# Kernel optimization log

Measured on AMD Instinct MI355X. Metric: run time of the kernel, lower is better.

## Reference

```python
import jax, jax.numpy as jnp
import numpy as np

V, D, K, NB, T = 50257, 128, 3, 8, 64
DIV_W = 2.0  # diversity_weight


def setup_inputs() -> dict:
    key = jax.random.key(0)
    k1, k2, k3 = jax.random.split(key, 3)
    tokens = jax.random.randint(k1, (T,), 0, V)
    E = jax.random.normal(k2, (V, D), jnp.float32)          # embedding table
    bubbles = 1.5 * jax.random.normal(k3, (K, NB, D), jnp.float32)  # init_spread_foam scale=1.5
    decay_base = jnp.asarray(0.8, jnp.float32)
    sensitivity = jnp.asarray(1.0, jnp.float32)
    return {"tokens": tokens, "E": E, "bubbles": bubbles,
            "decay_base": decay_base, "sensitivity": sensitivity}


def reference(tokens, E, bubbles, decay_base, sensitivity):
    d = E.shape[1]
    inv_sqrt_d = 1.0 / jnp.sqrt(jnp.asarray(d, jnp.float32))
    # normalized bubble states (pure-state directions), fixed over time
    psi = bubbles / (jnp.linalg.norm(bubbles, axis=-1, keepdims=True) + 1e-10)  # [K,NB,D]

    def step(memories, tok):
        # memories: [K, NB, D]
        x = E[tok]  # [D]
        mem_mean = memories.mean(axis=1)  # [K, D]
        mem_norm = jnp.linalg.norm(mem_mean, axis=-1) + 1e-10  # [K]
        x_norm = jnp.linalg.norm(x) + 1e-10
        cos = (mem_mean @ x) / (x_norm * mem_norm)  # [K]
        novelty = jnp.where(mem_norm > 1e-8, 1.0 - cos, 1.0)  # [K]
        decay = jax.nn.sigmoid(decay_base - jnp.abs(sensitivity) * novelty)  # [K]
        xm = x[None, :] + decay[:, None] * mem_mean  # [K, D]

        # foam forward (vectorized over K foams)
        scores = DIV_W * jnp.einsum('knd,kd->kn', bubbles, xm) * inv_sqrt_d  # [K,NB]
        w = jax.nn.softmax(scores, axis=-1)  # [K,NB]
        rho_k = jnp.einsum('kn,knd,kne->kde', w, psi, psi)  # [K,D,D] PSD, trace 1
        eq = w[..., None] * xm[:, None, :] + (1.0 - w)[..., None] * bubbles  # [K,NB,D]
        new_mem = decay[:, None, None] * memories + (1.0 - decay)[:, None, None] * eq

        rho = rho_k.mean(axis=0)  # [D,D] ensemble mixture
        eigs = jnp.clip(jnp.linalg.eigvalsh(rho), 1e-12)
        eigs = eigs / eigs.sum()
        logits = jnp.einsum('vd,de,ve->v', E, rho, E)  # born rule, [V]
        token_probs = jax.nn.softmax(logits)
        S_rho = -(eigs * jnp.clip(jnp.log(eigs), -100.0)).sum()
        H_tokens = -(token_probs * jnp.clip(jnp.log(token_probs), -100.0)).sum()
        F_tokens = H_tokens - S_rho
        logits_k = jnp.einsum('vd,kde,ve->kv', E, rho_k, E)  # [K,V]
        per_foam_probs = jax.nn.softmax(logits_k, axis=-1)
        return new_mem, (token_probs, rho, S_rho, H_tokens, F_tokens, per_foam_probs)

    mem0 = jnp.zeros((bubbles.shape[0], bubbles.shape[1], E.shape[1]), E.dtype)
    _, outs = jax.lax.scan(step, mem0, tokens)
    # outs: token_probs [T,V], rho [T,D,D], S_rho [T], H_tokens [T], F_tokens [T], per_foam_probs [T,K,V]
    return outs
```

## Files before the change

kernel.cpp:

```cpp
#include <hip/hip_runtime.h>
#include <math.h>

namespace {
constexpr int Vv  = 50257;
constexpr int Dc  = 128;
constexpr int Kc  = 3;
constexpr int NBc = 8;
constexpr int Jc  = 24;
constexpr int Tc  = 64;
constexpr int CHV = 1024;
constexpr int NCH = (Vv + CHV - 1) / CHV;
constexpr float INV_SQRT_D = 0.08838834764831845f;
constexpr float DIVW = 2.0f;

constexpr size_t WS_PSI  = 0;
constexpr size_t WS_G    = 4096;
constexpr size_t WS_BB   = 5120;
constexpr size_t WS_XN   = 6144;
constexpr size_t WS_BX   = 6400;
constexpr size_t WS_WALL = 8192;
constexpr size_t WS_PART = 12288;
constexpr size_t WS_LOGZ = 45056;
constexpr size_t WS_P2T  = 65536;

constexpr size_t OFF_TOK = 0;
constexpr size_t OFF_RHO = (size_t)Tc * Vv;
constexpr size_t OFF_S   = OFF_RHO + (size_t)Tc * Dc * Dc;
constexpr size_t OFF_H   = OFF_S + Tc;
constexpr size_t OFF_F   = OFF_H + Tc;
constexpr size_t OFF_PF  = OFF_F + Tc;
}

__device__ __forceinline__ float wsum64(float v) {
#pragma unroll
  for (int m = 1; m < 64; m <<= 1) v += __shfl_xor(v, m);
  return v;
}

__device__ __forceinline__ void comb(float& m1, float& s1, float m2, float s2) {
  float M = fmaxf(m1, m2);
  float e1 = (s1 > 0.f) ? expf(m1 - M) : 0.f;
  float e2 = (s2 > 0.f) ? expf(m2 - M) : 0.f;
  s1 = s1 * e1 + s2 * e2;
  m1 = M;
}
__device__ __forceinline__ void comb_sl(float& m1, float& s1, float& sl1,
                                        float m2, float s2, float sl2) {
  float M = fmaxf(m1, m2);
  float e1 = (s1 > 0.f) ? expf(m1 - M) : 0.f;
  float e2 = (s2 > 0.f) ? expf(m2 - M) : 0.f;
  s1 = s1 * e1 + s2 * e2;
  sl1 = sl1 * e1 + sl2 * e2;
  m1 = M;
}

__global__ void k_prep(const float* __restrict__ bub, float* __restrict__ ws) {
  __shared__ float braw[Jc * Dc];
  __shared__ float psi[Jc * Dc];
  __shared__ float nrm[Jc];
  int tid = threadIdx.x;
  for (int i = tid; i < Jc * Dc; i += 256) braw[i] = bub[i];
  __syncthreads();
  if (tid < Jc) {
    float s = 0.f;
    for (int d = 0; d < Dc; ++d) { float b = braw[tid * Dc + d]; s += b * b; }
    nrm[tid] = sqrtf(s) + 1e-10f;
  }
  __syncthreads();
  for (int i = tid; i < Jc * Dc; i += 256) {
    float v = braw[i] / nrm[i / Dc];
    psi[i] = v;
    ws[WS_PSI + i] = v;
  }
  __syncthreads();
  for (int i = tid; i < Jc * Jc; i += 256) {
    int r = i / Jc, c = i % Jc;
    float g = 0.f, b = 0.f;
    for (int d = 0; d < Dc; ++d) {
      g += psi[r * Dc + d] * psi[c * Dc + d];
      b += braw[r * Dc + d] * braw[c * Dc + d];
    }
    ws[WS_G + i] = g;
    ws[WS_BB + i] = b;
  }
}

__global__ void k_tok(const int* __restrict__ tok, const float* __restrict__ E,
                      const float* __restrict__ bub, float* __restrict__ ws) {
  int t = blockIdx.x, lane = threadIdx.x;
  int tk = tok[t];
  float eA = E[(size_t)tk * Dc + lane];
  float eB = E[(size_t)tk * Dc + 64 + lane];
  float xn = wsum64(eA * eA + eB * eB);
  if (lane == 0) ws[WS_XN + t] = xn;
  float p[Jc];
#pragma unroll
  for (int j = 0; j < Jc; ++j)
    p[j] = bub[j * Dc + lane] * eA + bub[j * Dc + 64 + lane] * eB;
#pragma unroll
  for (int j = 0; j < Jc; ++j) p[j] = wsum64(p[j]);
  if (lane == 0) {
#pragma unroll
    for (int j = 0; j < Jc; ++j) ws[WS_BX + (size_t)t * Jc + j] = p[j];
  }
}

__global__ void k_recur(const int* __restrict__ tok, const float* __restrict__ E,
                        const float* __restrict__ bub, const float* __restrict__ pdb,
                        const float* __restrict__ psn, float* __restrict__ ws) {
  __shared__ float sBX[Tc * Jc];
  __shared__ float sXN[Tc];
  int lane = threadIdx.x;
  for (int i = lane; i < Tc * Jc; i += 64) sBX[i] = ws[WS_BX + i];
  if (lane < Tc) sXN[lane] = ws[WS_XN + lane];
  float db = pdb[0];
  float sens = fabsf(psn[0]);
  int tokv = tok[lane];
  float bubA[Jc], bubB[Jc];
#pragma unroll
  for (int j = 0; j < Jc; ++j) {
    bubA[j] = bub[j * Dc + lane];
    bubB[j] = bub[j * Dc + 64 + lane];
  }
  int jme = (lane < Jc) ? lane : (Jc - 1);
  int kme = jme >> 3;
  float BBrow[Jc];
#pragma unroll
  for (int j = 0; j < Jc; ++j) BBrow[j] = ws[WS_BB + (size_t)jme * Jc + j];
  __syncthreads();
  float mmA[Kc] = {0.f, 0.f, 0.f}, mmB[Kc] = {0.f, 0.f, 0.f};
  float BMv[Kc] = {0.f, 0.f, 0.f};
  int tk0 = __shfl(tokv, 0);
  float xA = E[(size_t)tk0 * Dc + lane];
  float xB = E[(size_t)tk0 * Dc + 64 + lane];
  for (int t = 0; t < Tc; ++t) {
    float nxA = 0.f, nxB = 0.f;
    if (t + 1 < Tc) {
      int nk = __shfl(tokv, t + 1);
      nxA = E[(size_t)nk * Dc + lane];
      nxB = E[(size_t)nk * Dc + 64 + lane];
    }
    float dk[Kc], nk2[Kc];
#pragma unroll
    for (int k = 0; k < Kc; ++k) {
      dk[k]  = wsum64(mmA[k] * xA + mmB[k] * xB);
      nk2[k] = wsum64(mmA[k] * mmA[k] + mmB[k] * mmB[k]);
    }
    float xn = sqrtf(sXN[t]) + 1e-10f;
    float dec[Kc], xmA[Kc], xmB[Kc];
#pragma unroll
    for (int k = 0; k < Kc; ++k) {
      float mn = sqrtf(nk2[k]) + 1e-10f;
      float cosv = dk[k] / (xn * mn);
      float nov = (mn > 1e-8f) ? (1.f - cosv) : 1.f;
      dec[k] = 1.f / (1.f + expf(-(db - sens * nov)));
      xmA[k] = xA + dec[k] * mmA[k];
      xmB[k] = xB + dec[k] * mmB[k];
    }
    float bxj = sBX[t * Jc + jme];
    float decS = (kme == 0) ? dec[0] : ((kme == 1) ? dec[1] : dec[2]);
    float sc = (bxj + decS * BMv[kme]) * (DIVW * INV_SQRT_D);
    float mx = sc;
    mx = fmaxf(mx, __shfl_xor(mx, 1));
    mx = fmaxf(mx, __shfl_xor(mx, 2));
    mx = fmaxf(mx, __shfl_xor(mx, 4));
    float e = expf(sc - mx);
    float ss = e;
    ss += __shfl_xor(ss, 1);
    ss += __shfl_xor(ss, 2);
    ss += __shfl_xor(ss, 4);
    float w = e / ss;
    if (lane < Jc) ws[WS_WALL + (size_t)t * Jc + lane] = w;
    float wj[Jc];
#pragma unroll
    for (int j = 0; j < Jc; ++j) wj[j] = __shfl(w, j);
#pragma unroll
    for (int k = 0; k < Kc; ++k) {
      float accA = 0.f, accB = 0.f;
#pragma unroll
      for (int n = 0; n < NBc; ++n) {
        float om = 1.f - wj[k * NBc + n];
        accA += om * bubA[k * NBc + n];
        accB += om * bubB[k * NBc + n];
      }
      float od8 = (1.f - dec[k]) * 0.125f;
      mmA[k] = dec[k] * mmA[k] + od8 * (xmA[k] + accA);
      mmB[k] = dec[k] * mmB[k] + od8 * (xmB[k] + accB);
    }
#pragma unroll
    for (int k = 0; k < Kc; ++k) {
      float bxm = bxj + dec[k] * BMv[k];
      float s2 = 0.f;
#pragma unroll
      for (int n = 0; n < NBc; ++n) s2 += (1.f - wj[k * NBc + n]) * BBrow[k * NBc + n];
      BMv[k] = dec[k] * BMv[k] + (1.f - dec[k]) * 0.125f * (bxm + s2);
    }
    xA = nxA; xB = nxB;
  }
}

__global__ void k_proj(const float* __restrict__ E, float* __restrict__ ws) {
  __shared__ float4 psi4[Jc][Dc / 4];
  int tid = threadIdx.x;
  for (int i = tid; i < Jc * Dc / 4; i += 256)
    ((float4*)psi4)[i] = ((const float4*)(ws + WS_PSI))[i];
  __syncthreads();
  int v = blockIdx.x * 256 + tid;
  if (v >= Vv) return;
  float acc[Jc];
#pragma unroll
  for (int j = 0; j < Jc; ++j) acc[j] = 0.f;
  const float4* e4 = (const float4*)(E + (size_t)v * Dc);
  for (int d = 0; d < Dc / 4; ++d) {
    float4 e = e4[d];
#pragma unroll
    for (int j = 0; j < Jc; ++j) {
      float4 p = psi4[j][d];
      acc[j] += e.x * p.x + e.y * p.y + e.z * p.z + e.w * p.w;
    }
  }
#pragma unroll
  for (int j = 0; j < Jc; ++j) ws[WS_P2T + (size_t)j * Vv + v] = acc[j] * acc[j];
}

__global__ void k_rho(const float* __restrict__ ws, float* __restrict__ out) {
  int t = blockIdx.x;
  __shared__ float psis[Jc * Dc];
  __shared__ float wsh[Jc];
  int tid = threadIdx.x;
  for (int i = tid; i < Jc * Dc; i += 256) psis[i] = ws[WS_PSI + i];
  if (tid < Jc) wsh[tid] = ws[WS_WALL + (size_t)t * Jc + tid] * (1.f / 3.f);
  __syncthreads();
  int d = tid >> 1, eh = (tid & 1) * 64;
  float4 acc[16];
#pragma unroll
  for (int i = 0; i < 16; ++i) acc[i] = make_float4(0.f, 0.f, 0.f, 0.f);
  for (int j = 0; j < Jc; ++j) {
    float a = wsh[j] * psis[j * Dc + d];
    const float4* pr = (const float4*)&psis[j * Dc + eh];
#pragma unroll
    for (int i = 0; i < 16; ++i) {
      float4 p = pr[i];
      acc[i].x += a * p.x; acc[i].y += a * p.y; acc[i].z += a * p.z; acc[i].w += a * p.w;
    }
  }
  float* o = out + OFF_RHO + (size_t)t * Dc * Dc + (size_t)d * Dc + eh;
#pragma unroll
  for (int i = 0; i < 16; ++i) ((float4*)o)[i] = acc[i];
}

__global__ void k_eig(const float* __restrict__ ws, float* __restrict__ out) {
  int t = blockIdx.x;
  __shared__ float A[Jc * 25];
  int lane = threadIdx.x;
  for (int i = lane; i < Jc * Jc; i += 64) {
    int r = i / Jc, c = i % Jc;
    A[r * 25 + c] = ws[WS_G + i] *
                    sqrtf(ws[WS_WALL + (size_t)t * Jc + r] * ws[WS_WALL + (size_t)t * Jc + c]) *
                    (1.f / 3.f);
  }
  __syncthreads();
  for (int sweep = 0; sweep < 7; ++sweep) {
    for (int rr = 0; rr < 23; ++rr) {
      float cv = 1.f, sv = 0.f;
      if (lane < Jc) {
        int j = lane;
        int m = (j == 23) ? rr : ((j == rr) ? 23 : (2 * rr + 23 - j) % 23);
        int lo = min(j, m), hi = max(j, m);
        float ajj = A[j * 25 + j];
        float alh = A[lo * 25 + hi];
        float amm = __shfl(ajj, m);
        float app = (j == lo) ? ajj : amm;
        float aqq = (j == lo) ? amm : ajj;
        if (fabsf(alh) > 1e-20f) {
          float th = (aqq - app) / (2.f * alh);
          float tt = 1.f / (fabsf(th) + sqrtf(1.f + th * th));
          if (th < 0.f) tt = -tt;
          cv = 1.f / sqrtf(1.f + tt * tt);
          sv = tt * cv;
        }
      }
      __builtin_amdgcn_wave_barrier();
#pragma unroll
      for (int it = 0; it < 3; ++it) {
        int b = lane + 64 * it;
        int bb = (b < 144) ? b : 143;
        int pi = bb / 12, pj = bb % 12;
        int p0, q0, p1, q1;
        if (pi == 0) { p0 = rr; q0 = 23; }
        else { int a = (rr + pi) % 23, b2 = (rr + 23 - pi) % 23; p0 = min(a, b2); q0 = max(a, b2); }
        if (pj == 0) { p1 = rr; q1 = 23; }
        else { int a = (rr + pj) % 23, b2 = (rr + 23 - pj) % 23; p1 = min(a, b2); q1 = max(a, b2); }
        float ci = __shfl(cv, p0), si = __shfl(sv, p0);
        float cj = __shfl(cv, p1), sj = __shfl(sv, p1);
        if (b < 144) {
          float m00 = A[p0 * 25 + p1], m01 = A[p0 * 25 + q1];
          float m10 = A[q0 * 25 + p1], m11 = A[q0 * 25 + q1];
          float r00 = ci * m00 - si * m10, r01 = ci * m01 - si * m11;
          float r10 = si * m00 + ci * m10, r11 = si * m01 + ci * m11;
          float o00 = cj * r00 - sj * r01, o01 = sj * r00 + cj * r01;
          float o10 = cj * r10 - sj * r11, o11 = sj * r10 + cj * r11;
          A[p0 * 25 + p1] = o00; A[p0 * 25 + q1] = o01;
          A[q0 * 25 + p1] = o10; A[q0 * 25 + q1] = o11;
        }
      }
      __builtin_amdgcn_wave_barrier();
    }
  }
  float lam = 0.f;
  if (lane < Jc) lam = fmaxf(A[lane * 25 + lane], 1e-12f);
  float tot = lam;
#pragma unroll
  for (int off = 32; off; off >>= 1) tot += __shfl_down(tot, off);
  tot = __shfl(tot, 0);
  tot += (float)(Dc - Jc) * 1e-12f;
  float term = 0.f;
  if (lane < Jc) { float p = lam / tot; term = p * logf(p); }
#pragma unroll
  for (int off = 32; off; off >>= 1) term += __shfl_down(term, off);
  if (lane == 0) {
    float pe = 1e-12f / tot;
    out[OFF_S + t] = -(term + (float)(Dc - Jc) * pe * logf(pe));
  }
}

__global__ void k_logits(float* __restrict__ ws, float* __restrict__ out) {
  int ch = blockIdx.x, t = blockIdx.y, tid = threadIdx.x;
  __shared__ float wsh[Jc];
  __shared__ float rm[4][4], rs[4][4], rsl2[4];
  if (tid < Jc) wsh[tid] = ws[WS_WALL + (size_t)t * Jc + tid];
  __syncthreads();
  float m[4] = {-INFINITY, -INFINITY, -INFINITY, -INFINITY};
  float s[4] = {0.f, 0.f, 0.f, 0.f};
  float sl = 0.f;
  const float* p2 = ws + WS_P2T;
  for (int r = 0; r < 4; ++r) {
    int v = ch * CHV + r * 256 + tid;
    if (v >= Vv) break;
    float l0 = 0.f, l1 = 0.f, l2 = 0.f;
#pragma unroll
    for (int n = 0; n < NBc; ++n) {
      l0 += wsh[n]      * p2[(size_t)n * Vv + v];
      l1 += wsh[8 + n]  * p2[(size_t)(8 + n) * Vv + v];
      l2 += wsh[16 + n] * p2[(size_t)(16 + n) * Vv + v];
    }
    float l[4] = { l0, l1, l2, (l0 + l1 + l2) * (1.f / 3.f) };
    out[OFF_TOK + (size_t)t * Vv + v] = l[3];
    out[OFF_PF + ((size_t)t * Kc + 0) * Vv + v] = l0;
    out[OFF_PF + ((size_t)t * Kc + 1) * Vv + v] = l1;
    out[OFF_PF + ((size_t)t * Kc + 2) * Vv + v] = l2;
#pragma unroll
    for (int d = 0; d < 4; ++d) {
      float li = l[d];
      if (li > m[d]) {
        float e = expf(m[d] - li);
        s[d] = s[d] * e + 1.f;
        if (d == 3) sl = sl * e + li;
        m[d] = li;
      } else {
        float e = expf(li - m[d]);
        s[d] += e;
        if (d == 3) sl += e * li;
      }
    }
  }
#pragma unroll
  for (int off = 32; off; off >>= 1) {
#pragma unroll
    for (int d = 0; d < 3; ++d) {
      float om = __shfl_down(m[d], off);
      float os = __shfl_down(s[d], off);
      comb(m[d], s[d], om, os);
    }
    float om = __shfl_down(m[3], off);
    float os = __shfl_down(s[3], off);
    float osl = __shfl_down(sl, off);
    comb_sl(m[3], s[3], sl, om, os, osl);
  }
  int wv = tid >> 6, ln = tid & 63;
  if (ln == 0) {
#pragma unroll
    for (int d = 0; d < 4; ++d) { rm[wv][d] = m[d]; rs[wv][d] = s[d]; }
    rsl2[wv] = sl;
  }
  __syncthreads();
  if (tid == 0) {
    float* part = ws + WS_PART + ((size_t)t * NCH + ch) * 9;
    for (int d = 0; d < 3; ++d) {
      float M = rm[0][d], S = rs[0][d];
      for (int w2 = 1; w2 < 4; ++w2) comb(M, S, rm[w2][d], rs[w2][d]);
      part[d] = M; part[4 + d] = S;
    }
    float M = rm[0][3], S = rs[0][3], SL = rsl2[0];
    for (int w2 = 1; w2 < 4; ++w2) comb_sl(M, S, SL, rm[w2][3], rs[w2][3], rsl2[w2]);
    part[3] = M; part[7] = S; part[8] = SL;
  }
}

__global__ void k_reduce(float* __restrict__ ws, float* __restrict__ out) {
  int t = blockIdx.x, tid = threadIdx.x;
  if (tid < 4) {
    float M = -INFINITY, S = 0.f, SL = 0.f;
    for (int ch = 0; ch < NCH; ++ch) {
      const float* p = ws + WS_PART + ((size_t)t * NCH + ch) * 9;
      if (tid == 3) comb_sl(M, S, SL, p[3], p[7], p[8]);
      else          comb(M, S, p[tid], p[4 + tid]);
    }
    float lz = M + logf(S);
    ws[WS_LOGZ + (size_t)t * 4 + tid] = lz;
    if (tid == 3) {
      float H = lz - SL / S;
      float Srho = out[OFF_S + t];
      out[OFF_H + t] = H;
      out[OFF_F + t] = H - Srho;
    }
  }
}

__global__ void k_norm(const float* __restrict__ ws, float* __restrict__ out, int foam) {
  int row = blockIdx.y, ch = blockIdx.x, tid = threadIdx.x;
  size_t base; int lzi;
  if (foam) { int t = row / Kc, k = row % Kc; base = OFF_PF + (size_t)row * Vv; lzi = t * 4 + k; }
  else { base = OFF_TOK + (size_t)row * Vv; lzi = row * 4 + 3; }
  float lz = ws[WS_LOGZ + lzi];
  for (int r = 0; r < 4; ++r) {
    int v = ch * CHV + r * 256 + tid;
    if (v < Vv) out[base + v] = expf(out[base + v] - lz);
  }
}

extern "C" void kernel_launch(void* const* d_in, const int* in_sizes, int n_in,
                              void* d_out, int out_size, void* d_ws, size_t ws_size,
                              hipStream_t stream) {
  const int*   tokens = (const int*)d_in[0];
  const float* E      = (const float*)d_in[1];
  const float* bub    = (const float*)d_in[2];
  const float* pdb    = (const float*)d_in[3];
  const float* psn    = (const float*)d_in[4];
  float* out = (float*)d_out;
  float* ws  = (float*)d_ws;

  k_prep<<<1, 256, 0, stream>>>(bub, ws);
  k_proj<<<(Vv + 255) / 256, 256, 0, stream>>>(E, ws);
  k_tok<<<Tc, 64, 0, stream>>>(tokens, E, bub, ws);
  k_recur<<<1, 64, 0, stream>>>(tokens, E, bub, pdb, psn, ws);
  k_rho<<<Tc, 256, 0, stream>>>(ws, out);
  k_eig<<<Tc, 64, 0, stream>>>(ws, out);
  k_logits<<<dim3(NCH, Tc), 256, 0, stream>>>(ws, out);
  k_reduce<<<Tc, 64, 0, stream>>>(ws, out);
  k_norm<<<dim3(NCH, Tc), 256, 0, stream>>>(ws, out, 0);
  k_norm<<<dim3(NCH, Tc * Kc), 256, 0, stream>>>(ws, out, 1);
}
```

Measured before the change: 501.3 us.

## Replace two-sided Jacobi eigensolver with one-sided Jacobi on scaled psi columns in registers

The eigenvalue kernel no longer builds the 24x24 Gram-weighted matrix in shared memory and applies two-sided Jacobi rotations. It now runs a one-sided (Hestenes) Jacobi on the 24 weight-scaled psi vectors held in registers, two D-elements per lane. Each off-diagonal entry is computed with a wave reduction, and the rotation pairs are cycled through a round-robin register shuffle. This removes the shared-memory traffic and index arithmetic, but adds 12 wave reductions per rotation round, and diagonal norms are updated incrementally, which may drift numerically.

```diff
diff --git a/kernel.cpp b/kernel.cpp
--- a/kernel.cpp
+++ b/kernel.cpp
@@ -251,77 +251,60 @@
 
 __global__ void k_eig(const float* __restrict__ ws, float* __restrict__ out) {
   int t = blockIdx.x;
-  __shared__ float A[Jc * 25];
   int lane = threadIdx.x;
-  for (int i = lane; i < Jc * Jc; i += 64) {
-    int r = i / Jc, c = i % Jc;
-    A[r * 25 + c] = ws[WS_G + i] *
-                    sqrtf(ws[WS_WALL + (size_t)t * Jc + r] * ws[WS_WALL + (size_t)t * Jc + c]) *
-                    (1.f / 3.f);
-  }
-  __syncthreads();
+  float TA[12], TB[12], Tn[12], BA[12], BB[12], Bn[12];
+#pragma unroll
+  for (int i = 0; i < 12; ++i) {
+    int j0 = 2 * i, j1 = 2 * i + 1;
+    float w0 = ws[WS_WALL + (size_t)t * Jc + j0] * (1.f / 3.f);
+    float w1 = ws[WS_WALL + (size_t)t * Jc + j1] * (1.f / 3.f);
+    float s0 = sqrtf(w0), s1 = sqrtf(w1);
+    TA[i] = ws[WS_PSI + j0 * Dc + lane] * s0;
+    TB[i] = ws[WS_PSI + j0 * Dc + 64 + lane] * s0;
+    BA[i] = ws[WS_PSI + j1 * Dc + lane] * s1;
+    BB[i] = ws[WS_PSI + j1 * Dc + 64 + lane] * s1;
+    Tn[i] = w0; Bn[i] = w1;
+  }
   for (int sweep = 0; sweep < 7; ++sweep) {
     for (int rr = 0; rr < 23; ++rr) {
-      float cv = 1.f, sv = 0.f;
-      if (lane < Jc) {
-        int j = lane;
-        int m = (j == 23) ? rr : ((j == rr) ? 23 : (2 * rr + 23 - j) % 23);
-        int lo = min(j, m), hi = max(j, m);
-        float ajj = A[j * 25 + j];
-        float alh = A[lo * 25 + hi];
-        float amm = __shfl(ajj, m);
-        float app = (j == lo) ? ajj : amm;
-        float aqq = (j == lo) ? amm : ajj;
-        if (fabsf(alh) > 1e-20f) {
-          float th = (aqq - app) / (2.f * alh);
+#pragma unroll
+      for (int i = 0; i < 12; ++i) {
+        float apq = wsum64(TA[i] * BA[i] + TB[i] * BB[i]);
+        if (fabsf(apq) > 1e-11f) {
+          float app = Tn[i], aqq = Bn[i];
+          float th = (aqq - app) / (2.f * apq);
           float tt = 1.f / (fabsf(th) + sqrtf(1.f + th * th));
           if (th < 0.f) tt = -tt;
-          cv = 1.f / sqrtf(1.f + tt * tt);
-          sv = tt * cv;
+          float c = 1.f / sqrtf(1.f + tt * tt);
+          float s = tt * c;
+          float ta = TA[i], tb = TB[i], ba = BA[i], bb = BB[i];
+          TA[i] = c * ta - s * ba; BA[i] = s * ta + c * ba;
+          TB[i] = c * tb - s * bb; BB[i] = s * tb + c * bb;
+          Tn[i] = app - tt * apq;  Bn[i] = aqq + tt * apq;
         }
       }
-      __builtin_amdgcn_wave_barrier();
-#pragma unroll
-      for (int it = 0; it < 3; ++it) {
-        int b = lane + 64 * it;
-        int bb = (b < 144) ? b : 143;
-        int pi = bb / 12, pj = bb % 12;
-        int p0, q0, p1, q1;
-        if (pi == 0) { p0 = rr; q0 = 23; }
-        else { int a = (rr + pi) % 23, b2 = (rr + 23 - pi) % 23; p0 = min(a, b2); q0 = max(a, b2); }
-        if (pj == 0) { p1 = rr; q1 = 23; }
-        else { int a = (rr + pj) % 23, b2 = (rr + 23 - pj) % 23; p1 = min(a, b2); q1 = max(a, b2); }
-        float ci = __shfl(cv, p0), si = __shfl(sv, p0);
-        float cj = __shfl(cv, p1), sj = __shfl(sv, p1);
-        if (b < 144) {
-          float m00 = A[p0 * 25 + p1], m01 = A[p0 * 25 + q1];
-          float m10 = A[q0 * 25 + p1], m11 = A[q0 * 25 + q1];
-          float r00 = ci * m00 - si * m10, r01 = ci * m01 - si * m11;
-          float r10 = si * m00 + ci * m10, r11 = si * m01 + ci * m11;
-          float o00 = cj * r00 - sj * r01, o01 = sj * r00 + cj * r01;
-          float o10 = cj * r10 - sj * r11, o11 = sj * r10 + cj * r11;
-          A[p0 * 25 + p1] = o00; A[p0 * 25 + q1] = o01;
-          A[q0 * 25 + p1] = o10; A[q0 * 25 + q1] = o11;
-        }
-      }
-      __builtin_amdgcn_wave_barrier();
-    }
-  }
-  float lam = 0.f;
-  if (lane < Jc) lam = fmaxf(A[lane * 25 + lane], 1e-12f);
-  float tot = lam;
-#pragma unroll
-  for (int off = 32; off; off >>= 1) tot += __shfl_down(tot, off);
-  tot = __shfl(tot, 0);
+      float tA = TA[11], tB = TB[11], tN = Tn[11];
+#pragma unroll
+      for (int i = 11; i >= 2; --i) { TA[i] = TA[i-1]; TB[i] = TB[i-1]; Tn[i] = Tn[i-1]; }
+      TA[1] = BA[0]; TB[1] = BB[0]; Tn[1] = Bn[0];
+#pragma unroll
+      for (int i = 0; i <= 10; ++i) { BA[i] = BA[i+1]; BB[i] = BB[i+1]; Bn[i] = Bn[i+1]; }
+      BA[11] = tA; BB[11] = tB; Bn[11] = tN;
+    }
+  }
+  float lam[Jc];
+#pragma unroll
+  for (int i = 0; i < 12; ++i) { lam[i] = fmaxf(Tn[i], 1e-12f); lam[12 + i] = fmaxf(Bn[i], 1e-12f); }
+  float tot = 0.f;
+#pragma unroll
+  for (int i = 0; i < Jc; ++i) tot += lam[i];
   tot += (float)(Dc - Jc) * 1e-12f;
-  float term = 0.f;
-  if (lane < Jc) { float p = lam / tot; term = p * logf(p); }
-#pragma unroll
-  for (int off = 32; off; off >>= 1) term += __shfl_down(term, off);
-  if (lane == 0) {
-    float pe = 1e-12f / tot;
-    out[OFF_S + t] = -(term + (float)(Dc - Jc) * pe * logf(pe));
-  }
+  float acc = 0.f;
+#pragma unroll
+  for (int i = 0; i < Jc; ++i) { float p = lam[i] / tot; acc += p * logf(p); }
+  float pe = 1e-12f / tot;
+  acc += (float)(Dc - Jc) * pe * logf(pe);
+  if (lane == 0) out[OFF_S + t] = -acc;
 }
 
 __global__ void k_logits(float* __restrict__ ws, float* __restrict__ out) {
```

Result: slower. 1.121 ms (+123.6%).
